# Performance work log

Hardware: AMD Instinct MI355X
Metric: run time of the kernel (lower is better)

## Reference

```python
import jax, jax.numpy as jnp
import numpy as np
from jax import lax

N_NODES, N_EDGES, N_GRAPHS = 102400, 409600, 2048
HID, BN_EPS = 128, 1e-5


def setup_inputs():
    kit = iter(jax.random.split(jax.random.key(0), 64))

    def nrm(shape, s=0.02):
        return jax.random.normal(next(kit), shape, jnp.float32) * s

    inp = {}
    inp["x_ligand"] = jax.random.normal(next(kit), (N_NODES, 78), jnp.float32)
    inp["protein_seq"] = jax.random.normal(next(kit), (N_GRAPHS, 1, 1000), jnp.float32)
    inp["a2h"] = jax.random.normal(next(kit), (N_GRAPHS, 10, 100, 3), jnp.float32)
    inp["edge_index"] = jax.random.randint(next(kit), (2, N_EDGES), 0, N_NODES)
    inp["batch_ligand"] = jnp.sort(jax.random.randint(next(kit), (N_NODES,), 0, N_GRAPHS))
    dins = [78, HID, HID]
    for i in range(3):
        inp[f"gin{i}_W1"] = nrm((dins[i], HID)); inp[f"gin{i}_b1"] = jnp.zeros((HID,), jnp.float32)
        inp[f"gin{i}_W2"] = nrm((HID, HID)); inp[f"gin{i}_b2"] = jnp.zeros((HID,), jnp.float32)
        inp[f"bn{i}_g"] = jnp.ones((HID,), jnp.float32); inp[f"bn{i}_b"] = jnp.zeros((HID,), jnp.float32)
    inp["lig_W"] = nrm((HID, HID)); inp["lig_b"] = jnp.zeros((HID,), jnp.float32)
    inp["conv_k"] = nrm((32, 1, 8)); inp["conv_b"] = jnp.zeros((32,), jnp.float32)
    inp["prot_W"] = nrm((32, HID)); inp["prot_b"] = jnp.zeros((HID,), jnp.float32)
    inp["a2h1_W"] = nrm((3000, HID)); inp["a2h1_b"] = jnp.zeros((HID,), jnp.float32)
    inp["a2h2_W"] = nrm((HID, HID)); inp["a2h2_b"] = jnp.zeros((HID,), jnp.float32)
    inp["c1_W"] = nrm((3 * HID, 2 * HID)); inp["c1_b"] = jnp.zeros((2 * HID,), jnp.float32)
    inp["c2_W"] = nrm((2 * HID, HID)); inp["c2_b"] = jnp.zeros((HID,), jnp.float32)
    inp["out_W"] = nrm((HID, 1)); inp["out_b"] = jnp.zeros((1,), jnp.float32)
    return inp


def _gin_layer(x, src, dst, W1, b1, W2, b2, g, b):
    # scatter-add neighbor aggregation (PyG GINConv, eps=0)
    agg = jax.ops.segment_sum(x[src], dst, num_segments=N_NODES)
    h = x + agg
    h = jax.nn.relu(h @ W1 + b1) @ W2 + b2  # GIN MLP
    mu = h.mean(0)
    var = h.var(0)
    h = (h - mu) * lax.rsqrt(var + BN_EPS) * g + b  # BatchNorm1d (batch stats)
    return jax.nn.relu(h)


def _forward(x_ligand, protein_seq, a2h, edge_index, batch_ligand, gin_params,
             lig_W, lig_b, conv_k, conv_b, prot_W, prot_b,
             a2h1_W, a2h1_b, a2h2_W, a2h2_b, c1_W, c1_b, c2_W, c2_b, out_W, out_b):
    src, dst = edge_index[0], edge_index[1]
    x = x_ligand
    for (W1, b1, W2, b2, g, b) in gin_params:
        x = _gin_layer(x, src, dst, W1, b1, W2, b2, g, b)
    xg = jax.ops.segment_sum(x, batch_ligand, num_segments=N_GRAPHS)  # global_add_pool
    xg = jax.nn.relu(xg @ lig_W + lig_b)
    # protein CNN branch: Conv1d(1->32, k=8) + ReLU + global max pool
    xp = lax.conv_general_dilated(protein_seq, conv_k, (1,), 'VALID',
                                  dimension_numbers=('NCH', 'OIH', 'NCH')) + conv_b[None, :, None]
    xp = jax.nn.relu(xp).max(axis=-1)
    xp = jax.nn.relu(xp @ prot_W + prot_b)
    # a2h MLP branch on flattened trajectory
    xa = a2h.reshape(a2h.shape[0], -1)
    xa = jax.nn.relu(xa @ a2h1_W + a2h1_b)
    xa = jax.nn.relu(xa @ a2h2_W + a2h2_b)
    xc = jnp.concatenate([xg, xp, xa], axis=1)
    xc = jax.nn.relu(xc @ c1_W + c1_b)
    xc = jax.nn.relu(xc @ c2_W + c2_b)
    return xc @ out_W + out_b


def reference(x_ligand, protein_seq, a2h, edge_index, batch_ligand,
              gin0_W1, gin0_b1, gin0_W2, gin0_b2, bn0_g, bn0_b,
              gin1_W1, gin1_b1, gin1_W2, gin1_b2, bn1_g, bn1_b,
              gin2_W1, gin2_b1, gin2_W2, gin2_b2, bn2_g, bn2_b,
              lig_W, lig_b, conv_k, conv_b, prot_W, prot_b,
              a2h1_W, a2h1_b, a2h2_W, a2h2_b, c1_W, c1_b, c2_W, c2_b, out_W, out_b):
    gin_params = [
        (gin0_W1, gin0_b1, gin0_W2, gin0_b2, bn0_g, bn0_b),
        (gin1_W1, gin1_b1, gin1_W2, gin1_b2, bn1_g, bn1_b),
        (gin2_W1, gin2_b1, gin2_W2, gin2_b2, bn2_g, bn2_b),
    ]
    return _forward(x_ligand, protein_seq, a2h, edge_index, batch_ligand, gin_params,
                    lig_W, lig_b, conv_k, conv_b, prot_W, prot_b,
                    a2h1_W, a2h1_b, a2h2_W, a2h2_b, c1_W, c1_b, c2_W, c2_b, out_W, out_b)
```

## Files before the change

### kernel.cpp

```cpp
#include <hip/hip_runtime.h>
#include <math.h>

constexpr int NNODES  = 102400;
constexpr int NEDGES  = 409600;
constexpr int NGRAPHS = 2048;
constexpr int HIDDEN  = 128;

__device__ __forceinline__ float relu_f(float v) { return fmaxf(v, 0.0f); }

__global__ void hist2_kernel(const int* __restrict__ ei, const int* __restrict__ batch,
                             int* __restrict__ counts, int* __restrict__ gcounts) {
  int b = blockIdx.x;
  if (b < NEDGES / 256) {
    int e = b * 256 + threadIdx.x;
    atomicAdd(&counts[ei[NEDGES + e]], 1);
  } else {
    int i = (b - NEDGES / 256) * 256 + threadIdx.x;
    atomicAdd(&gcounts[batch[i]], 1);
  }
}

__device__ __forceinline__ void scan_block_body(const int* in, int n, int* out_excl,
                                                int* bsums, int lb) {
  __shared__ int s[256];
  int t = threadIdx.x;
  int i = lb * 256 + t;
  int v = (i < n) ? in[i] : 0;
  s[t] = v;
  __syncthreads();
  for (int off = 1; off < 256; off <<= 1) {
    int x = (t >= off) ? s[t - off] : 0;
    __syncthreads();
    s[t] += x;
    __syncthreads();
  }
  if (i < n) out_excl[i] = s[t] - v;
  if (t == 255) bsums[lb] = s[255];
}

__global__ void scan_block2_kernel(const int* __restrict__ counts, int* __restrict__ row_ptr,
                                   int* __restrict__ bsumsA, const int* __restrict__ gcounts,
                                   int* __restrict__ gptr, int* __restrict__ bsumsB) {
  int b = blockIdx.x;
  if (b < NNODES / 256) scan_block_body(counts, NNODES, row_ptr, bsumsA, b);
  else scan_block_body(gcounts, NGRAPHS, gptr, bsumsB, b - NNODES / 256);
}

__global__ void scan_top2_kernel(int* __restrict__ bsumsA, int* __restrict__ bsumsB) {
  __shared__ int s[1024];
  int* bs = (blockIdx.x == 0) ? bsumsA : bsumsB;
  int nb  = (blockIdx.x == 0) ? (NNODES / 256) : (NGRAPHS / 256);
  int t = threadIdx.x;
  int v = (t < nb) ? bs[t] : 0;
  s[t] = v;
  __syncthreads();
  for (int off = 1; off < 1024; off <<= 1) {
    int x = (t >= off) ? s[t - off] : 0;
    __syncthreads();
    s[t] += x;
    __syncthreads();
  }
  if (t < nb) bs[t] = s[t] - v;
  if (t == 1023) bs[nb] = s[1023];
}

__global__ void scan_add2_kernel(int* __restrict__ row_ptr, const int* __restrict__ bsumsA,
                                 int* __restrict__ nxt, int* __restrict__ gptr,
                                 const int* __restrict__ bsumsB) {
  int b = blockIdx.x, t = threadIdx.x;
  if (b < NNODES / 256) {
    int i = b * 256 + t;
    int v = row_ptr[i] + bsumsA[b];
    row_ptr[i] = v;
    nxt[i] = v;
    if (i == 0) row_ptr[NNODES] = bsumsA[NNODES / 256];
  } else {
    int lb = b - NNODES / 256;
    int i = lb * 256 + t;
    gptr[i] += bsumsB[lb];
    if (i == 0) gptr[NGRAPHS] = bsumsB[NGRAPHS / 256];
  }
}

__global__ void scatter_kernel(const int* __restrict__ ei, int* __restrict__ nxt,
                               int* __restrict__ csr_src) {
  int e = blockIdx.x * blockDim.x + threadIdx.x;
  if (e < NEDGES) {
    int s = ei[e];
    int d = ei[NEDGES + e];
    int pos = atomicAdd(&nxt[d], 1);
    csr_src[pos] = s;
  }
}

template<int DIN, bool XF>
__device__ __forceinline__ void gin_block(
    int bid, const float* __restrict__ X,
    const int* __restrict__ row_ptr, const int* __restrict__ csr_src,
    const float* __restrict__ W1, const float* __restrict__ b1,
    const float* __restrict__ W2, const float* __restrict__ b2,
    const float* __restrict__ psum, const float* __restrict__ psq,
    const float* __restrict__ bg, const float* __restrict__ bb2,
    float* __restrict__ O, float* __restrict__ bn_sum, float* __restrict__ bn_sq,
    float* buf) {
  constexpr int R = 32, STR = R + 4;
  const int t = threadIdx.x;
  const int wv = t >> 6, lane = t & 63;
  const int base = bid * R;

  const int fp = 2 * lane;
  if (fp < DIN) {
    float sc0 = 1.f, sh0 = 0.f, sc1 = 1.f, sh1 = 0.f;
    if (XF) {
      float mu0 = psum[fp] * (1.0f / NNODES);
      float va0 = fmaxf(psq[fp] * (1.0f / NNODES) - mu0 * mu0, 0.0f);
      sc0 = bg[fp] / sqrtf(va0 + 1e-5f);
      sh0 = bb2[fp] - mu0 * sc0;
      float mu1 = psum[fp + 1] * (1.0f / NNODES);
      float va1 = fmaxf(psq[fp + 1] * (1.0f / NNODES) - mu1 * mu1, 0.0f);
      sc1 = bg[fp + 1] / sqrtf(va1 + 1e-5f);
      sh1 = bb2[fp + 1] - mu1 * sc1;
    }
    for (int g = 0; g < 2; ++g) {
      const int rbase = wv * 8 + g * 4;
      float a0[4], a1[4];
      int ecur[4], eend[4], idx[4];
#pragma unroll
      for (int r = 0; r < 4; ++r) {
        const int node = base + rbase + r;
        ecur[r] = row_ptr[node];
        eend[r] = row_ptr[node + 1];
        const float2 s = *(const float2*)&X[(long)node * DIN + fp];
        a0[r] = XF ? relu_f(fmaf(s.x, sc0, sh0)) : s.x;
        a1[r] = XF ? relu_f(fmaf(s.y, sc1, sh1)) : s.y;
        idx[r] = (ecur[r] < eend[r]) ? csr_src[ecur[r]] : -1;
      }
      bool any = (idx[0] >= 0) || (idx[1] >= 0) || (idx[2] >= 0) || (idx[3] >= 0);
      while (any) {
        float2 uu[4];
#pragma unroll
        for (int r = 0; r < 4; ++r)
          if (idx[r] >= 0) uu[r] = *(const float2*)&X[(long)idx[r] * DIN + fp];
        any = false;
#pragma unroll
        for (int r = 0; r < 4; ++r) {
          if (idx[r] >= 0) {
            a0[r] += XF ? relu_f(fmaf(uu[r].x, sc0, sh0)) : uu[r].x;
            a1[r] += XF ? relu_f(fmaf(uu[r].y, sc1, sh1)) : uu[r].y;
            ++ecur[r];
            idx[r] = (ecur[r] < eend[r]) ? csr_src[ecur[r]] : -1;
          }
          any = any || (idx[r] >= 0);
        }
      }
#pragma unroll
      for (int r = 0; r < 4; ++r) {
        buf[fp * STR + rbase + r] = a0[r];
        buf[(fp + 1) * STR + rbase + r] = a1[r];
      }
    }
  }
  __syncthreads();

  const int rg = t >> 5, cg = t & 31;
  const int r0 = rg * 4, j0 = cg * 4;

  float acc[4][4];
  {
    const float4 bbv = *(const float4*)&b1[j0];
    for (int r = 0; r < 4; ++r) { acc[r][0]=bbv.x; acc[r][1]=bbv.y; acc[r][2]=bbv.z; acc[r][3]=bbv.w; }
    for (int k = 0; k < DIN; ++k) {
      const float4 w = *(const float4*)&W1[k * HIDDEN + j0];
      const float4 x = *(const float4*)&buf[k * STR + r0];
      const float xa[4] = {x.x, x.y, x.z, x.w};
      const float wa[4] = {w.x, w.y, w.z, w.w};
      for (int r = 0; r < 4; ++r)
        for (int c = 0; c < 4; ++c)
          acc[r][c] = fmaf(xa[r], wa[c], acc[r][c]);
    }
  }
  __syncthreads();

  for (int c = 0; c < 4; ++c) {
    float4 m = { relu_f(acc[0][c]), relu_f(acc[1][c]), relu_f(acc[2][c]), relu_f(acc[3][c]) };
    *(float4*)&buf[(j0 + c) * STR + r0] = m;
  }
  __syncthreads();

  float csum[4] = {0,0,0,0}, csq[4] = {0,0,0,0};
  {
    const float4 bbv = *(const float4*)&b2[j0];
    for (int r = 0; r < 4; ++r) { acc[r][0]=bbv.x; acc[r][1]=bbv.y; acc[r][2]=bbv.z; acc[r][3]=bbv.w; }
    for (int k = 0; k < HIDDEN; ++k) {
      const float4 w = *(const float4*)&W2[k * HIDDEN + j0];
      const float4 x = *(const float4*)&buf[k * STR + r0];
      const float xa[4] = {x.x, x.y, x.z, x.w};
      const float wa[4] = {w.x, w.y, w.z, w.w};
      for (int r = 0; r < 4; ++r)
        for (int c = 0; c < 4; ++c)
          acc[r][c] = fmaf(xa[r], wa[c], acc[r][c]);
    }
    for (int r = 0; r < 4; ++r) {
      float4 o = { acc[r][0], acc[r][1], acc[r][2], acc[r][3] };
      *(float4*)&O[(long)(base + r0 + r) * HIDDEN + j0] = o;
      for (int c = 0; c < 4; ++c) {
        csum[c] += acc[r][c];
        csq[c] = fmaf(acc[r][c], acc[r][c], csq[c]);
      }
    }
  }
  __syncthreads();
  for (int c = 0; c < 4; ++c) {
    buf[(j0 + c) * 8 + rg] = csum[c];
    buf[1024 + (j0 + c) * 8 + rg] = csq[c];
  }
  __syncthreads();
  if (t < HIDDEN) {
    float s = 0.f, q = 0.f;
    for (int g = 0; g < 8; ++g) { s += buf[t * 8 + g]; q += buf[1024 + t * 8 + g]; }
    atomicAdd(&bn_sum[t], s);
    atomicAdd(&bn_sq[t], q);
  }
}

constexpr int A2H_K = 3000, A2H_SPLIT = 200, A2H_NSPLIT = 15;
__device__ __forceinline__ void a2h_block(int rb, int sp, const float* __restrict__ A,
    const float* __restrict__ W, const float* __restrict__ bias, float* __restrict__ XA,
    float* xT) {
  constexpr int STR = 18;
  const int t = threadIdx.x;
  const int row0 = rb * 16;
  const int k0 = sp * A2H_SPLIT;
  for (int i = t; i < 16 * 50; i += 256) {
    const int r = i / 50, kq = i - r * 50;
    const float4 v = *(const float4*)&A[(long)(row0 + r) * A2H_K + k0 + kq * 4];
    xT[(kq * 4 + 0) * STR + r] = v.x;
    xT[(kq * 4 + 1) * STR + r] = v.y;
    xT[(kq * 4 + 2) * STR + r] = v.z;
    xT[(kq * 4 + 3) * STR + r] = v.w;
  }
  __syncthreads();
  const int rg = t >> 5, cg = t & 31;
  const int r0 = rg * 2, j0 = cg * 4;
  float acc[2][4];
  for (int r = 0; r < 2; ++r)
    for (int c = 0; c < 4; ++c) acc[r][c] = 0.f;
  const float* Wp = W + (long)k0 * HIDDEN + j0;
  for (int k = 0; k < A2H_SPLIT; ++k) {
    const float4 w = *(const float4*)&Wp[(long)k * HIDDEN];
    const float2 x = *(const float2*)&xT[k * STR + r0];
    const float wa[4] = {w.x, w.y, w.z, w.w};
    for (int c = 0; c < 4; ++c) {
      acc[0][c] = fmaf(x.x, wa[c], acc[0][c]);
      acc[1][c] = fmaf(x.y, wa[c], acc[1][c]);
    }
  }
  if (sp == 0)
    for (int c = 0; c < 4; ++c) { acc[0][c] += bias[j0 + c]; acc[1][c] += bias[j0 + c]; }
  for (int r = 0; r < 2; ++r)
    for (int c = 0; c < 4; ++c)
      atomicAdd(&XA[(long)(row0 + r0 + r) * HIDDEN + j0 + c], acc[r][c]);
}

__device__ __forceinline__ void conv_block(int g, const float* __restrict__ PS,
    const float* __restrict__ CK, const float* __restrict__ CB, float* __restrict__ XP,
    float* seq) {
  const int t = threadIdx.x;
  for (int i = t; i < 1000; i += 256) seq[i] = PS[g * 1000 + i];
  __syncthreads();
  const int pl = t & 31, cgp = t >> 5;
  float kr[4][8];
  for (int cc = 0; cc < 4; ++cc)
    for (int k = 0; k < 8; ++k) kr[cc][k] = CK[(cgp * 4 + cc) * 8 + k];
  float m[4] = {-1e30f, -1e30f, -1e30f, -1e30f};
  for (int i = 0; i < 32; ++i) {
    int p = pl + 32 * i;
    if (p < 993) {
      float sv[8];
      for (int k = 0; k < 8; ++k) sv[k] = seq[p + k];
      for (int cc = 0; cc < 4; ++cc) {
        float s = 0.f;
        for (int k = 0; k < 8; ++k) s = fmaf(sv[k], kr[cc][k], s);
        m[cc] = fmaxf(m[cc], s);
      }
    }
  }
  for (int off = 16; off >= 1; off >>= 1)
    for (int cc = 0; cc < 4; ++cc) m[cc] = fmaxf(m[cc], __shfl_xor(m[cc], off));
  if (pl == 0)
    for (int cc = 0; cc < 4; ++cc)
      XP[g * 32 + cgp * 4 + cc] = relu_f(m[cc] + CB[cgp * 4 + cc]);
}

__global__ __launch_bounds__(256, 8) void fat0_kernel(
    const float* __restrict__ x_lig, const int* __restrict__ row_ptr,
    const int* __restrict__ csr_src,
    const float* __restrict__ W1, const float* __restrict__ b1,
    const float* __restrict__ W2, const float* __restrict__ b2,
    float* __restrict__ O0, float* __restrict__ bn_sum, float* __restrict__ bn_sq,
    const float* __restrict__ a2h, const float* __restrict__ a1W,
    const float* __restrict__ a1b, float* __restrict__ XA,
    const float* __restrict__ pseq, const float* __restrict__ convk,
    const float* __restrict__ convb, float* __restrict__ XP32) {
  __shared__ __align__(16) float buf[128 * 36];
  const int b = blockIdx.x;
  if (b < NNODES / 32) {
    gin_block<78, false>(b, x_lig, row_ptr, csr_src, W1, b1, W2, b2,
                         nullptr, nullptr, nullptr, nullptr, O0, bn_sum, bn_sq, buf);
  } else if (b < NNODES / 32 + (NGRAPHS / 16) * A2H_NSPLIT) {
    const int q = b - NNODES / 32;
    a2h_block(q & 127, q >> 7, a2h, a1W, a1b, XA, buf);
  } else {
    conv_block(b - (NNODES / 32 + (NGRAPHS / 16) * A2H_NSPLIT), pseq, convk, convb, XP32, buf);
  }
}

template<int DIN, bool XF>
__global__ __launch_bounds__(256, 8) void gin_kernel(
    const float* __restrict__ X, const int* __restrict__ row_ptr,
    const int* __restrict__ csr_src,
    const float* __restrict__ W1, const float* __restrict__ b1,
    const float* __restrict__ W2, const float* __restrict__ b2,
    const float* __restrict__ psum, const float* __restrict__ psq,
    const float* __restrict__ bg, const float* __restrict__ bb2,
    float* __restrict__ O, float* __restrict__ bn_sum, float* __restrict__ bn_sq) {
  __shared__ __align__(16) float buf[128 * 36];
  gin_block<DIN, XF>(blockIdx.x, X, row_ptr, csr_src, W1, b1, W2, b2,
                     psum, psq, bg, bb2, O, bn_sum, bn_sq, buf);
}

__global__ __launch_bounds__(256) void pool_kernel(const float* __restrict__ O,
    const int* __restrict__ gp, const float* __restrict__ psum, const float* __restrict__ psq,
    const float* __restrict__ bg, const float* __restrict__ bb2, float* __restrict__ P) {
  int t = threadIdx.x;
  int g = blockIdx.x * 4 + (t >> 6);
  int lane = t & 63;
  int f0 = lane, f1 = lane + 64;
  float mu0 = psum[f0] * (1.0f / NNODES);
  float va0 = fmaxf(psq[f0] * (1.0f / NNODES) - mu0 * mu0, 0.0f);
  float sc0 = bg[f0] / sqrtf(va0 + 1e-5f);
  float sh0 = bb2[f0] - mu0 * sc0;
  float mu1 = psum[f1] * (1.0f / NNODES);
  float va1 = fmaxf(psq[f1] * (1.0f / NNODES) - mu1 * mu1, 0.0f);
  float sc1 = bg[f1] / sqrtf(va1 + 1e-5f);
  float sh1 = bb2[f1] - mu1 * sc1;
  int n0 = gp[g], n1 = gp[g + 1];
  float a0 = 0.f, a1 = 0.f;
  for (int n = n0; n < n1; ++n) {
    a0 += relu_f(fmaf(O[(long)n * HIDDEN + f0], sc0, sh0));
    a1 += relu_f(fmaf(O[(long)n * HIDDEN + f1], sc1, sh1));
  }
  P[g * HIDDEN + f0] = a0;
  P[g * HIDDEN + f1] = a1;
}

__device__ __forceinline__ void gemm16_body(const float* __restrict__ A, int lda, int K,
    const float* __restrict__ W, int ldw, const float* __restrict__ bias,
    float* __restrict__ C, int ldc, int coff, int yc, bool reluA, float* AT) {
  constexpr int RT = 16, CH = 64, STR = RT + 4;
  const int t = threadIdx.x;
  const int rg = t >> 6, cg = t & 63;
  const int r0 = rg * 4;
  const int row0 = blockIdx.x * RT;
  const int col = yc * 64 + cg;
  float a0 = 0.f, a1 = 0.f, a2 = 0.f, a3 = 0.f;
  for (int k0 = 0; k0 < K; k0 += CH) {
    const int kc = min(CH, K - k0);
    __syncthreads();
    for (int i = t; i < RT * CH; i += 256) {
      int kk = i & (CH - 1), r = i >> 6;
      if (kk < kc) {
        float v = A[(long)(row0 + r) * lda + k0 + kk];
        AT[kk * STR + r] = reluA ? relu_f(v) : v;
      }
    }
    __syncthreads();
    for (int kk = 0; kk < kc; ++kk) {
      const float4 x = *(const float4*)&AT[kk * STR + r0];
      const float w = W[(long)(k0 + kk) * ldw + col];
      a0 = fmaf(x.x, w, a0);
      a1 = fmaf(x.y, w, a1);
      a2 = fmaf(x.z, w, a2);
      a3 = fmaf(x.w, w, a3);
    }
  }
  const float bv = bias[col];
  C[(long)(row0 + r0 + 0) * ldc + coff + col] = relu_f(a0 + bv);
  C[(long)(row0 + r0 + 1) * ldc + coff + col] = relu_f(a1 + bv);
  C[(long)(row0 + r0 + 2) * ldc + coff + col] = relu_f(a2 + bv);
  C[(long)(row0 + r0 + 3) * ldc + coff + col] = relu_f(a3 + bv);
}

__global__ __launch_bounds__(256) void branches_kernel(
    const float* __restrict__ P, const float* __restrict__ XP32, const float* __restrict__ XA,
    const float* __restrict__ ligW, const float* __restrict__ ligb,
    const float* __restrict__ protW, const float* __restrict__ protb,
    const float* __restrict__ a2W, const float* __restrict__ a2b, float* __restrict__ XC) {
  __shared__ __align__(16) float AT[64 * 20];
  const int cfg = blockIdx.y >> 1, yc = blockIdx.y & 1;
  if (cfg == 0)      gemm16_body(P,    128, 128, ligW,  128, ligb,  XC, 384, 0,   yc, false, AT);
  else if (cfg == 1) gemm16_body(XP32, 32,  32,  protW, 128, protb, XC, 384, 128, yc, false, AT);
  else               gemm16_body(XA,   128, 128, a2W,   128, a2b,   XC, 384, 256, yc, true,  AT);
}

__global__ __launch_bounds__(256) void gemm2_kernel(const float* __restrict__ A, int lda, int K,
    const float* __restrict__ W, int ldw, const float* __restrict__ bias,
    float* __restrict__ C, int ldc) {
  __shared__ __align__(16) float AT[64 * 20];
  gemm16_body(A, lda, K, W, ldw, bias, C, ldc, 0, blockIdx.y, false, AT);
}

__global__ __launch_bounds__(256) void final_dot_kernel(const float* __restrict__ X,
    const float* __restrict__ Wo, const float* __restrict__ bo, float* __restrict__ out) {
  int t = threadIdx.x;
  int g = blockIdx.x * 4 + (t >> 6);
  int lane = t & 63;
  float2 x = *(const float2*)&X[g * HIDDEN + lane * 2];
  float2 w = *(const float2*)&Wo[lane * 2];
  float p = x.x * w.x + x.y * w.y;
  for (int off = 32; off >= 1; off >>= 1) p += __shfl_down(p, off);
  if (lane == 0) out[g] = p + bo[0];
}

extern "C" void kernel_launch(void* const* d_in, const int* in_sizes, int n_in,
                              void* d_out, int out_size, void* d_ws, size_t ws_size,
                              hipStream_t stream) {
  const float* x_lig = (const float*)d_in[0];
  const float* pseq  = (const float*)d_in[1];
  const float* a2h   = (const float*)d_in[2];
  const int*   ei    = (const int*)d_in[3];
  const int*   batch = (const int*)d_in[4];
  const float* ginW1[3] = {(const float*)d_in[5],  (const float*)d_in[11], (const float*)d_in[17]};
  const float* ginb1[3] = {(const float*)d_in[6],  (const float*)d_in[12], (const float*)d_in[18]};
  const float* ginW2[3] = {(const float*)d_in[7],  (const float*)d_in[13], (const float*)d_in[19]};
  const float* ginb2[3] = {(const float*)d_in[8],  (const float*)d_in[14], (const float*)d_in[20]};
  const float* bng[3]   = {(const float*)d_in[9],  (const float*)d_in[15], (const float*)d_in[21]};
  const float* bnb[3]   = {(const float*)d_in[10], (const float*)d_in[16], (const float*)d_in[22]};
  const float* ligW  = (const float*)d_in[23]; const float* ligb  = (const float*)d_in[24];
  const float* convk = (const float*)d_in[25]; const float* convb = (const float*)d_in[26];
  const float* protW = (const float*)d_in[27]; const float* protb = (const float*)d_in[28];
  const float* a1W   = (const float*)d_in[29]; const float* a1b   = (const float*)d_in[30];
  const float* a2W   = (const float*)d_in[31]; const float* a2b   = (const float*)d_in[32];
  const float* c1W   = (const float*)d_in[33]; const float* c1b   = (const float*)d_in[34];
  const float* c2W   = (const float*)d_in[35]; const float* c2b   = (const float*)d_in[36];
  const float* oW    = (const float*)d_in[37]; const float* ob    = (const float*)d_in[38];

  char* base = (char*)d_ws;
  size_t off = 0;
  auto alloc = [&](size_t bytes) -> char* {
    char* p = base + off;
    off = (off + bytes + 511) & ~size_t(511);
    return p;
  };
  int*   counts  = (int*)alloc(NNODES * 4);
  int*   gcounts = (int*)alloc(NGRAPHS * 4);
  float* bn_sum  = (float*)alloc(3 * 128 * 4);
  float* bn_sq   = (float*)alloc(3 * 128 * 4);
  float* XA      = (float*)alloc(NGRAPHS * 128 * 4);
  const size_t zero_bytes = off;
  int*   row_ptr  = (int*)alloc((NNODES + 1) * 4);
  int*   nxt      = (int*)alloc(NNODES * 4);
  int*   gptr     = (int*)alloc((NGRAPHS + 1) * 4);
  int*   bsumsA   = (int*)alloc(401 * 4);
  int*   bsumsB   = (int*)alloc(9 * 4);
  int*   csr_src  = (int*)alloc(NEDGES * 4);
  float* P        = (float*)alloc(NGRAPHS * 128 * 4);
  float* XP32     = (float*)alloc(NGRAPHS * 32 * 4);
  float* XC       = (float*)alloc(NGRAPHS * 384 * 4);
  float* XC2      = (float*)alloc(NGRAPHS * 256 * 4);
  float* XC3      = (float*)alloc(NGRAPHS * 128 * 4);
  float* O0       = (float*)alloc((size_t)NNODES * 128 * 4);
  float* O1       = (float*)alloc((size_t)NNODES * 128 * 4);
  (void)ws_size; (void)in_sizes; (void)n_in; (void)out_size;

  hipMemsetAsync(d_ws, 0, zero_bytes, stream);

  hist2_kernel<<<NEDGES / 256 + NNODES / 256, 256, 0, stream>>>(ei, batch, counts, gcounts);
  scan_block2_kernel<<<NNODES / 256 + NGRAPHS / 256, 256, 0, stream>>>(
      counts, row_ptr, bsumsA, gcounts, gptr, bsumsB);
  scan_top2_kernel<<<2, 1024, 0, stream>>>(bsumsA, bsumsB);
  scan_add2_kernel<<<NNODES / 256 + NGRAPHS / 256, 256, 0, stream>>>(
      row_ptr, bsumsA, nxt, gptr, bsumsB);
  scatter_kernel<<<(NEDGES + 255) / 256, 256, 0, stream>>>(ei, nxt, csr_src);

  fat0_kernel<<<NNODES / 32 + (NGRAPHS / 16) * A2H_NSPLIT + NGRAPHS, 256, 0, stream>>>(
      x_lig, row_ptr, csr_src, ginW1[0], ginb1[0], ginW2[0], ginb2[0],
      O0, bn_sum, bn_sq, a2h, a1W, a1b, XA, pseq, convk, convb, XP32);

  gin_kernel<128, true><<<NNODES / 32, 256, 0, stream>>>(O0, row_ptr, csr_src,
      ginW1[1], ginb1[1], ginW2[1], ginb2[1], bn_sum, bn_sq, bng[0], bnb[0],
      O1, bn_sum + 128, bn_sq + 128);
  gin_kernel<128, true><<<NNODES / 32, 256, 0, stream>>>(O1, row_ptr, csr_src,
      ginW1[2], ginb1[2], ginW2[2], ginb2[2], bn_sum + 128, bn_sq + 128, bng[1], bnb[1],
      O0, bn_sum + 256, bn_sq + 256);

  pool_kernel<<<NGRAPHS / 4, 256, 0, stream>>>(O0, gptr, bn_sum + 256, bn_sq + 256,
                                               bng[2], bnb[2], P);
  branches_kernel<<<dim3(NGRAPHS / 16, 6), 256, 0, stream>>>(
      P, XP32, XA, ligW, ligb, protW, protb, a2W, a2b, XC);
  gemm2_kernel<<<dim3(NGRAPHS / 16, 4), 256, 0, stream>>>(XC, 384, 384, c1W, 256, c1b, XC2, 256);
  gemm2_kernel<<<dim3(NGRAPHS / 16, 2), 256, 0, stream>>>(XC2, 256, 256, c2W, 128, c2b, XC3, 128);
  final_dot_kernel<<<NGRAPHS / 4, 256, 0, stream>>>(XC3, oW, ob, (float*)d_out);
}
```

Before: 880.9 us.

## Run GIN MLP matmuls on bf16 MFMA with three-way split for fp32 accuracy

Replaces the scalar FP32 FMA loops of both GIN MLP layers with bf16 MFMA 16x16x32 instructions. Activations and weights are each split into three bf16 pieces and six cross products are accumulated to approximate fp32 precision. Weights are pre-split once into an MFMA-friendly layout by extending the histogram kernel. The shared-memory tile becomes row-major with padding, and launch bounds drop from 8 to 4 blocks per CU, which may lower occupancy for the gather-bound aggregation phase.

```diff
diff --git a/kernel.cpp b/kernel.cpp
--- a/kernel.cpp
+++ b/kernel.cpp
@@ -6,18 +6,56 @@
 constexpr int NGRAPHS = 2048;
 constexpr int HIDDEN  = 128;
 
+typedef __attribute__((ext_vector_type(8))) short s16x8;
+typedef __attribute__((ext_vector_type(4))) float f32x4;
+
 __device__ __forceinline__ float relu_f(float v) { return fmaxf(v, 0.0f); }
 
-__global__ void hist2_kernel(const int* __restrict__ ei, const int* __restrict__ batch,
-                             int* __restrict__ counts, int* __restrict__ gcounts) {
+__device__ __forceinline__ void split3(float x, short& s0, short& s1, short& s2) {
+  unsigned u0 = __float_as_uint(x);
+  s0 = (short)(u0 >> 16);
+  float r1 = x - __uint_as_float(u0 & 0xFFFF0000u);
+  unsigned u1 = __float_as_uint(r1);
+  s1 = (short)(u1 >> 16);
+  float r2 = r1 - __uint_as_float(u1 & 0xFFFF0000u);
+  s2 = (short)(__float_as_uint(r2) >> 16);
+}
+
+__global__ void prep_kernel(const int* __restrict__ ei, const int* __restrict__ batch,
+                            int* __restrict__ counts, int* __restrict__ gcounts,
+                            const float* __restrict__ W10, const float* __restrict__ W20,
+                            const float* __restrict__ W11, const float* __restrict__ W21,
+                            const float* __restrict__ W12, const float* __restrict__ W22,
+                            short* __restrict__ ws) {
   int b = blockIdx.x;
   if (b < NEDGES / 256) {
-    int e = b * 256 + threadIdx.x;
-    atomicAdd(&counts[ei[NEDGES + e]], 1);
+    atomicAdd(&counts[ei[NEDGES + b * 256 + threadIdx.x]], 1);
+    return;
+  }
+  if (b < NEDGES / 256 + NNODES / 256) {
+    atomicAdd(&gcounts[batch[(b - NEDGES / 256) * 256 + threadIdx.x]], 1);
+    return;
+  }
+  int bw = b - (NEDGES / 256 + NNODES / 256);
+  int n = threadIdx.x;
+  if (n >= 128) return;
+  const float* src; long base; int k, realK, KP;
+  if (bw < 96) {
+    src = W10; base = 0; k = bw; realK = 78; KP = 96;
   } else {
-    int i = (b - NEDGES / 256) * 256 + threadIdx.x;
-    atomicAdd(&gcounts[batch[i]], 1);
-  }
+    int q = bw - 96;
+    int mat = q >> 7;
+    k = q & 127; realK = 128; KP = 128;
+    const float* srcs[5] = {W20, W11, W21, W12, W22};
+    const long bases[5] = {36864, 86016, 135168, 184320, 233472};
+    src = srcs[mat]; base = bases[mat];
+  }
+  float x = (k < realK) ? src[k * 128 + n] : 0.0f;
+  short s0, s1, s2;
+  split3(x, s0, s1, s2);
+  long e = base + ((long)(k >> 5) * 128 + n) * 32 + (k & 31);
+  long ps = (long)KP * 128;
+  ws[e] = s0; ws[e + ps] = s1; ws[e + 2 * ps] = s2;
 }
 
 __device__ __forceinline__ void scan_block_body(const int* in, int n, int* out_excl,
@@ -93,131 +131,201 @@
   }
 }
 
-template<int DIN, bool XF>
+constexpr int STRK = 132;
+template<int DIN, int KP1, bool XF>
 __device__ __forceinline__ void gin_block(
     int bid, const float* __restrict__ X,
     const int* __restrict__ row_ptr, const int* __restrict__ csr_src,
-    const float* __restrict__ W1, const float* __restrict__ b1,
-    const float* __restrict__ W2, const float* __restrict__ b2,
+    const short* __restrict__ w1s, const float* __restrict__ b1,
+    const short* __restrict__ w2s, const float* __restrict__ b2,
     const float* __restrict__ psum, const float* __restrict__ psq,
     const float* __restrict__ bg, const float* __restrict__ bb2,
     float* __restrict__ O, float* __restrict__ bn_sum, float* __restrict__ bn_sq,
     float* buf) {
-  constexpr int R = 32, STR = R + 4;
   const int t = threadIdx.x;
   const int wv = t >> 6, lane = t & 63;
-  const int base = bid * R;
+  const int base = bid * 32;
 
   const int fp = 2 * lane;
-  if (fp < DIN) {
-    float sc0 = 1.f, sh0 = 0.f, sc1 = 1.f, sh1 = 0.f;
-    if (XF) {
-      float mu0 = psum[fp] * (1.0f / NNODES);
-      float va0 = fmaxf(psq[fp] * (1.0f / NNODES) - mu0 * mu0, 0.0f);
-      sc0 = bg[fp] / sqrtf(va0 + 1e-5f);
-      sh0 = bb2[fp] - mu0 * sc0;
-      float mu1 = psum[fp + 1] * (1.0f / NNODES);
-      float va1 = fmaxf(psq[fp + 1] * (1.0f / NNODES) - mu1 * mu1, 0.0f);
-      sc1 = bg[fp + 1] / sqrtf(va1 + 1e-5f);
-      sh1 = bb2[fp + 1] - mu1 * sc1;
-    }
-    for (int g = 0; g < 2; ++g) {
-      const int rbase = wv * 8 + g * 4;
-      float a0[4], a1[4];
-      int ecur[4], eend[4], idx[4];
-#pragma unroll
-      for (int r = 0; r < 4; ++r) {
-        const int node = base + rbase + r;
-        ecur[r] = row_ptr[node];
-        eend[r] = row_ptr[node + 1];
-        const float2 s = *(const float2*)&X[(long)node * DIN + fp];
-        a0[r] = XF ? relu_f(fmaf(s.x, sc0, sh0)) : s.x;
-        a1[r] = XF ? relu_f(fmaf(s.y, sc1, sh1)) : s.y;
-        idx[r] = (ecur[r] < eend[r]) ? csr_src[ecur[r]] : -1;
+  if (fp < KP1) {
+    if (fp < DIN) {
+      float sc0 = 1.f, sh0 = 0.f, sc1 = 1.f, sh1 = 0.f;
+      if (XF) {
+        float mu0 = psum[fp] * (1.0f / NNODES);
+        float va0 = fmaxf(psq[fp] * (1.0f / NNODES) - mu0 * mu0, 0.0f);
+        sc0 = bg[fp] / sqrtf(va0 + 1e-5f);
+        sh0 = bb2[fp] - mu0 * sc0;
+        float mu1 = psum[fp + 1] * (1.0f / NNODES);
+        float va1 = fmaxf(psq[fp + 1] * (1.0f / NNODES) - mu1 * mu1, 0.0f);
+        sc1 = bg[fp + 1] / sqrtf(va1 + 1e-5f);
+        sh1 = bb2[fp + 1] - mu1 * sc1;
       }
-      bool any = (idx[0] >= 0) || (idx[1] >= 0) || (idx[2] >= 0) || (idx[3] >= 0);
-      while (any) {
-        float2 uu[4];
+      for (int g = 0; g < 2; ++g) {
+        const int rbase = wv * 8 + g * 4;
+        float a0[4], a1[4];
+        int ecur[4], eend[4], idx[4];
+#pragma unroll
+        for (int r = 0; r < 4; ++r) {
+          const int node = base + rbase + r;
+          ecur[r] = row_ptr[node];
+          eend[r] = row_ptr[node + 1];
+          const float2 s = *(const float2*)&X[(long)node * DIN + fp];
+          a0[r] = XF ? relu_f(fmaf(s.x, sc0, sh0)) : s.x;
+          a1[r] = XF ? relu_f(fmaf(s.y, sc1, sh1)) : s.y;
+          idx[r] = (ecur[r] < eend[r]) ? csr_src[ecur[r]] : -1;
+        }
+        bool any = (idx[0] >= 0) || (idx[1] >= 0) || (idx[2] >= 0) || (idx[3] >= 0);
+        while (any) {
+          float2 uu[4];
+#pragma unroll
+          for (int r = 0; r < 4; ++r)
+            if (idx[r] >= 0) uu[r] = *(const float2*)&X[(long)idx[r] * DIN + fp];
+          any = false;
+#pragma unroll
+          for (int r = 0; r < 4; ++r) {
+            if (idx[r] >= 0) {
+              a0[r] += XF ? relu_f(fmaf(uu[r].x, sc0, sh0)) : uu[r].x;
+              a1[r] += XF ? relu_f(fmaf(uu[r].y, sc1, sh1)) : uu[r].y;
+              ++ecur[r];
+              idx[r] = (ecur[r] < eend[r]) ? csr_src[ecur[r]] : -1;
+            }
+            any = any || (idx[r] >= 0);
+          }
+        }
 #pragma unroll
         for (int r = 0; r < 4; ++r)
-          if (idx[r] >= 0) uu[r] = *(const float2*)&X[(long)idx[r] * DIN + fp];
-        any = false;
-#pragma unroll
-        for (int r = 0; r < 4; ++r) {
-          if (idx[r] >= 0) {
-            a0[r] += XF ? relu_f(fmaf(uu[r].x, sc0, sh0)) : uu[r].x;
-            a1[r] += XF ? relu_f(fmaf(uu[r].y, sc1, sh1)) : uu[r].y;
-            ++ecur[r];
-            idx[r] = (ecur[r] < eend[r]) ? csr_src[ecur[r]] : -1;
-          }
-          any = any || (idx[r] >= 0);
-        }
+          *(float2*)&buf[(rbase + r) * STRK + fp] = make_float2(a0[r], a1[r]);
       }
-#pragma unroll
-      for (int r = 0; r < 4; ++r) {
-        buf[fp * STR + rbase + r] = a0[r];
-        buf[(fp + 1) * STR + rbase + r] = a1[r];
+    } else {
+      for (int r = 0; r < 8; ++r)
+        *(float2*)&buf[(wv * 8 + r) * STRK + fp] = make_float2(0.f, 0.f);
+    }
+  }
+  __syncthreads();
+
+  const int rb = wv & 1, nbase = (wv >> 1) * 64;
+  const int l15 = lane & 15, quad = lane >> 4;
+  const int aoff = (rb * 16 + l15) * STRK;
+  constexpr int PS1 = KP1 * 128;
+  constexpr int PS2 = 128 * 128;
+
+  f32x4 acc1[4] = {};
+  for (int ks = 0; ks < KP1 / 32; ++ks) {
+    const int k0 = ks * 32;
+    const float4 xa = *(const float4*)&buf[aoff + k0 + quad * 8];
+    const float4 xb = *(const float4*)&buf[aoff + k0 + quad * 8 + 4];
+    s16x8 A0, A1, A2;
+    {
+      const float xv[8] = {xa.x, xa.y, xa.z, xa.w, xb.x, xb.y, xb.z, xb.w};
+#pragma unroll
+      for (int j = 0; j < 8; ++j) {
+        short s0, s1, s2;
+        split3(xv[j], s0, s1, s2);
+        A0[j] = s0; A1[j] = s1; A2[j] = s2;
       }
     }
-  }
-  __syncthreads();
-
-  const int rg = t >> 5, cg = t & 31;
-  const int r0 = rg * 4, j0 = cg * 4;
-
-  float acc[4][4];
-  {
-    const float4 bbv = *(const float4*)&b1[j0];
-    for (int r = 0; r < 4; ++r) { acc[r][0]=bbv.x; acc[r][1]=bbv.y; acc[r][2]=bbv.z; acc[r][3]=bbv.w; }
-    for (int k = 0; k < DIN; ++k) {
-      const float4 w = *(const float4*)&W1[k * HIDDEN + j0];
-      const float4 x = *(const float4*)&buf[k * STR + r0];
-      const float xa[4] = {x.x, x.y, x.z, x.w};
-      const float wa[4] = {w.x, w.y, w.z, w.w};
-      for (int r = 0; r < 4; ++r)
-        for (int c = 0; c < 4; ++c)
-          acc[r][c] = fmaf(xa[r], wa[c], acc[r][c]);
-    }
-  }
-  __syncthreads();
-
-  for (int c = 0; c < 4; ++c) {
-    float4 m = { relu_f(acc[0][c]), relu_f(acc[1][c]), relu_f(acc[2][c]), relu_f(acc[3][c]) };
-    *(float4*)&buf[(j0 + c) * STR + r0] = m;
-  }
-  __syncthreads();
-
-  float csum[4] = {0,0,0,0}, csq[4] = {0,0,0,0};
-  {
-    const float4 bbv = *(const float4*)&b2[j0];
-    for (int r = 0; r < 4; ++r) { acc[r][0]=bbv.x; acc[r][1]=bbv.y; acc[r][2]=bbv.z; acc[r][3]=bbv.w; }
-    for (int k = 0; k < HIDDEN; ++k) {
-      const float4 w = *(const float4*)&W2[k * HIDDEN + j0];
-      const float4 x = *(const float4*)&buf[k * STR + r0];
-      const float xa[4] = {x.x, x.y, x.z, x.w};
-      const float wa[4] = {w.x, w.y, w.z, w.w};
-      for (int r = 0; r < 4; ++r)
-        for (int c = 0; c < 4; ++c)
-          acc[r][c] = fmaf(xa[r], wa[c], acc[r][c]);
-    }
-    for (int r = 0; r < 4; ++r) {
-      float4 o = { acc[r][0], acc[r][1], acc[r][2], acc[r][3] };
-      *(float4*)&O[(long)(base + r0 + r) * HIDDEN + j0] = o;
-      for (int c = 0; c < 4; ++c) {
-        csum[c] += acc[r][c];
-        csq[c] = fmaf(acc[r][c], acc[r][c], csq[c]);
+    s16x8 B0[4], B1[4], B2[4];
+#pragma unroll
+    for (int ct = 0; ct < 4; ++ct) {
+      const int n = nbase + ct * 16 + l15;
+      const short* wp = w1s + ((long)(ks * 128 + n) << 5) + (quad << 3);
+      B0[ct] = *(const s16x8*)(wp);
+      B1[ct] = *(const s16x8*)(wp + PS1);
+      B2[ct] = *(const s16x8*)(wp + 2 * PS1);
+    }
+#pragma unroll
+    for (int ct = 0; ct < 4; ++ct) acc1[ct] = __builtin_amdgcn_mfma_f32_16x16x32_bf16(A0, B2[ct], acc1[ct], 0, 0, 0);
+#pragma unroll
+    for (int ct = 0; ct < 4; ++ct) acc1[ct] = __builtin_amdgcn_mfma_f32_16x16x32_bf16(A1, B1[ct], acc1[ct], 0, 0, 0);
+#pragma unroll
+    for (int ct = 0; ct < 4; ++ct) acc1[ct] = __builtin_amdgcn_mfma_f32_16x16x32_bf16(A2, B0[ct], acc1[ct], 0, 0, 0);
+#pragma unroll
+    for (int ct = 0; ct < 4; ++ct) acc1[ct] = __builtin_amdgcn_mfma_f32_16x16x32_bf16(A0, B1[ct], acc1[ct], 0, 0, 0);
+#pragma unroll
+    for (int ct = 0; ct < 4; ++ct) acc1[ct] = __builtin_amdgcn_mfma_f32_16x16x32_bf16(A1, B0[ct], acc1[ct], 0, 0, 0);
+#pragma unroll
+    for (int ct = 0; ct < 4; ++ct) acc1[ct] = __builtin_amdgcn_mfma_f32_16x16x32_bf16(A0, B0[ct], acc1[ct], 0, 0, 0);
+  }
+  __syncthreads();
+
+#pragma unroll
+  for (int ct = 0; ct < 4; ++ct) {
+    const int n = nbase + ct * 16 + l15;
+    const float bb = b1[n];
+#pragma unroll
+    for (int reg = 0; reg < 4; ++reg) {
+      const int m = rb * 16 + quad * 4 + reg;
+      buf[m * STRK + n] = relu_f(acc1[ct][reg] + bb);
+    }
+  }
+  __syncthreads();
+
+  f32x4 acc2[4] = {};
+  for (int ks = 0; ks < 4; ++ks) {
+    const int k0 = ks * 32;
+    const float4 xa = *(const float4*)&buf[aoff + k0 + quad * 8];
+    const float4 xb = *(const float4*)&buf[aoff + k0 + quad * 8 + 4];
+    s16x8 A0, A1, A2;
+    {
+      const float xv[8] = {xa.x, xa.y, xa.z, xa.w, xb.x, xb.y, xb.z, xb.w};
+#pragma unroll
+      for (int j = 0; j < 8; ++j) {
+        short s0, s1, s2;
+        split3(xv[j], s0, s1, s2);
+        A0[j] = s0; A1[j] = s1; A2[j] = s2;
       }
     }
-  }
-  __syncthreads();
-  for (int c = 0; c < 4; ++c) {
-    buf[(j0 + c) * 8 + rg] = csum[c];
-    buf[1024 + (j0 + c) * 8 + rg] = csq[c];
+    s16x8 B0[4], B1[4], B2[4];
+#pragma unroll
+    for (int ct = 0; ct < 4; ++ct) {
+      const int n = nbase + ct * 16 + l15;
+      const short* wp = w2s + ((long)(ks * 128 + n) << 5) + (quad << 3);
+      B0[ct] = *(const s16x8*)(wp);
+      B1[ct] = *(const s16x8*)(wp + PS2);
+      B2[ct] = *(const s16x8*)(wp + 2 * PS2);
+    }
+#pragma unroll
+    for (int ct = 0; ct < 4; ++ct) acc2[ct] = __builtin_amdgcn_mfma_f32_16x16x32_bf16(A0, B2[ct], acc2[ct], 0, 0, 0);
+#pragma unroll
+    for (int ct = 0; ct < 4; ++ct) acc2[ct] = __builtin_amdgcn_mfma_f32_16x16x32_bf16(A1, B1[ct], acc2[ct], 0, 0, 0);
+#pragma unroll
+    for (int ct = 0; ct < 4; ++ct) acc2[ct] = __builtin_amdgcn_mfma_f32_16x16x32_bf16(A2, B0[ct], acc2[ct], 0, 0, 0);
+#pragma unroll
+    for (int ct = 0; ct < 4; ++ct) acc2[ct] = __builtin_amdgcn_mfma_f32_16x16x32_bf16(A0, B1[ct], acc2[ct], 0, 0, 0);
+#pragma unroll
+    for (int ct = 0; ct < 4; ++ct) acc2[ct] = __builtin_amdgcn_mfma_f32_16x16x32_bf16(A1, B0[ct], acc2[ct], 0, 0, 0);
+#pragma unroll
+    for (int ct = 0; ct < 4; ++ct) acc2[ct] = __builtin_amdgcn_mfma_f32_16x16x32_bf16(A0, B0[ct], acc2[ct], 0, 0, 0);
+  }
+
+  float cs[4], cq[4];
+#pragma unroll
+  for (int ct = 0; ct < 4; ++ct) {
+    const int n = nbase + ct * 16 + l15;
+    const float bb = b2[n];
+    float s = 0.f, q = 0.f;
+#pragma unroll
+    for (int reg = 0; reg < 4; ++reg) {
+      const int m = rb * 16 + quad * 4 + reg;
+      const float o = acc2[ct][reg] + bb;
+      O[(long)(base + m) * HIDDEN + n] = o;
+      s += o;
+      q = fmaf(o, o, q);
+    }
+    cs[ct] = s; cq[ct] = q;
+  }
+  __syncthreads();
+  const int g = rb * 4 + quad;
+#pragma unroll
+  for (int ct = 0; ct < 4; ++ct) {
+    const int n = nbase + ct * 16 + l15;
+    buf[n * 8 + g] = cs[ct];
+    buf[1024 + n * 8 + g] = cq[ct];
   }
   __syncthreads();
   if (t < HIDDEN) {
     float s = 0.f, q = 0.f;
-    for (int g = 0; g < 8; ++g) { s += buf[t * 8 + g]; q += buf[1024 + t * 8 + g]; }
+    for (int gg = 0; gg < 8; ++gg) { s += buf[t * 8 + gg]; q += buf[1024 + t * 8 + gg]; }
     atomicAdd(&bn_sum[t], s);
     atomicAdd(&bn_sq[t], q);
   }
@@ -292,21 +400,21 @@
       XP[g * 32 + cgp * 4 + cc] = relu_f(m[cc] + CB[cgp * 4 + cc]);
 }
 
-__global__ __launch_bounds__(256, 8) void fat0_kernel(
+__global__ __launch_bounds__(256, 4) void fat0_kernel(
     const float* __restrict__ x_lig, const int* __restrict__ row_ptr,
     const int* __restrict__ csr_src,
-    const float* __restrict__ W1, const float* __restrict__ b1,
-    const float* __restrict__ W2, const float* __restrict__ b2,
+    const short* __restrict__ ws, const float* __restrict__ b1,
+    const float* __restrict__ b2,
     float* __restrict__ O0, float* __restrict__ bn_sum, float* __restrict__ bn_sq,
     const float* __restrict__ a2h, const float* __restrict__ a1W,
     const float* __restrict__ a1b, float* __restrict__ XA,
     const float* __restrict__ pseq, const float* __restrict__ convk,
     const float* __restrict__ convb, float* __restrict__ XP32) {
-  __shared__ __align__(16) float buf[128 * 36];
+  __shared__ __align__(16) float buf[32 * STRK];
   const int b = blockIdx.x;
   if (b < NNODES / 32) {
-    gin_block<78, false>(b, x_lig, row_ptr, csr_src, W1, b1, W2, b2,
-                         nullptr, nullptr, nullptr, nullptr, O0, bn_sum, bn_sq, buf);
+    gin_block<78, 96, false>(b, x_lig, row_ptr, csr_src, ws, b1, ws + 36864, b2,
+                             nullptr, nullptr, nullptr, nullptr, O0, bn_sum, bn_sq, buf);
   } else if (b < NNODES / 32 + (NGRAPHS / 16) * A2H_NSPLIT) {
     const int q = b - NNODES / 32;
     a2h_block(q & 127, q >> 7, a2h, a1W, a1b, XA, buf);
@@ -315,18 +423,17 @@
   }
 }
 
-template<int DIN, bool XF>
-__global__ __launch_bounds__(256, 8) void gin_kernel(
+__global__ __launch_bounds__(256, 4) void gin_kernel(
     const float* __restrict__ X, const int* __restrict__ row_ptr,
     const int* __restrict__ csr_src,
-    const float* __restrict__ W1, const float* __restrict__ b1,
-    const float* __restrict__ W2, const float* __restrict__ b2,
+    const short* __restrict__ w1s, const float* __restrict__ b1,
+    const short* __restrict__ w2s, const float* __restrict__ b2,
     const float* __restrict__ psum, const float* __restrict__ psq,
     const float* __restrict__ bg, const float* __restrict__ bb2,
     float* __restrict__ O, float* __restrict__ bn_sum, float* __restrict__ bn_sq) {
-  __shared__ __align__(16) float buf[128 * 36];
-  gin_block<DIN, XF>(blockIdx.x, X, row_ptr, csr_src, W1, b1, W2, b2,
-                     psum, psq, bg, bb2, O, bn_sum, bn_sq, buf);
+  __shared__ __align__(16) float buf[32 * STRK];
+  gin_block<128, 128, true>(blockIdx.x, X, row_ptr, csr_src, w1s, b1, w2s, b2,
+                            psum, psq, bg, bb2, O, bn_sum, bn_sq, buf);
 }
 
 __global__ __launch_bounds__(256) void pool_kernel(const float* __restrict__ O,
@@ -458,6 +565,7 @@
   float* bn_sq   = (float*)alloc(3 * 128 * 4);
   float* XA      = (float*)alloc(NGRAPHS * 128 * 4);
   const size_t zero_bytes = off;
+  short* wsplit   = (short*)alloc(282624 * 2);
   int*   row_ptr  = (int*)alloc((NNODES + 1) * 4);
   int*   nxt      = (int*)alloc(NNODES * 4);
   int*   gptr     = (int*)alloc((NGRAPHS + 1) * 4);
@@ -475,7 +583,9 @@
 
   hipMemsetAsync(d_ws, 0, zero_bytes, stream);
 
-  hist2_kernel<<<NEDGES / 256 + NNODES / 256, 256, 0, stream>>>(ei, batch, counts, gcounts);
+  prep_kernel<<<NEDGES / 256 + NNODES / 256 + 736, 256, 0, stream>>>(
+      ei, batch, counts, gcounts, ginW1[0], ginW2[0], ginW1[1], ginW2[1],
+      ginW1[2], ginW2[2], wsplit);
   scan_block2_kernel<<<NNODES / 256 + NGRAPHS / 256, 256, 0, stream>>>(
       counts, row_ptr, bsumsA, gcounts, gptr, bsumsB);
   scan_top2_kernel<<<2, 1024, 0, stream>>>(bsumsA, bsumsB);
@@ -484,15 +594,15 @@
   scatter_kernel<<<(NEDGES + 255) / 256, 256, 0, stream>>>(ei, nxt, csr_src);
 
   fat0_kernel<<<NNODES / 32 + (NGRAPHS / 16) * A2H_NSPLIT + NGRAPHS, 256, 0, stream>>>(
-      x_lig, row_ptr, csr_src, ginW1[0], ginb1[0], ginW2[0], ginb2[0],
+      x_lig, row_ptr, csr_src, wsplit, ginb1[0], ginb2[0],
       O0, bn_sum, bn_sq, a2h, a1W, a1b, XA, pseq, convk, convb, XP32);
 
-  gin_kernel<128, true><<<NNODES / 32, 256, 0, stream>>>(O0, row_ptr, csr_src,
-      ginW1[1], ginb1[1], ginW2[1], ginb2[1], bn_sum, bn_sq, bng[0], bnb[0],
-      O1, bn_sum + 128, bn_sq + 128);
-  gin_kernel<128, true><<<NNODES / 32, 256, 0, stream>>>(O1, row_ptr, csr_src,
-      ginW1[2], ginb1[2], ginW2[2], ginb2[2], bn_sum + 128, bn_sq + 128, bng[1], bnb[1],
-      O0, bn_sum + 256, bn_sq + 256);
+  gin_kernel<<<NNODES / 32, 256, 0, stream>>>(O0, row_ptr, csr_src,
+      wsplit + 86016, ginb1[1], wsplit + 135168, ginb2[1],
+      bn_sum, bn_sq, bng[0], bnb[0], O1, bn_sum + 128, bn_sq + 128);
+  gin_kernel<<<NNODES / 32, 256, 0, stream>>>(O1, row_ptr, csr_src,
+      wsplit + 184320, ginb1[2], wsplit + 233472, ginb2[2],
+      bn_sum + 128, bn_sq + 128, bng[1], bnb[1], O0, bn_sum + 256, bn_sq + 256);
 
   pool_kernel<<<NGRAPHS / 4, 256, 0, stream>>>(O0, gptr, bn_sum + 256, bn_sq + 256,
                                                bng[2], bnb[2], P);
```

Result: faster. 848.3 us (-3.7%).
